# Kernel optimization log

Hardware: AMD Instinct MI355X
Metric: run time of the kernel (lower is better)

Reference implementation:

```python
import jax, jax.numpy as jnp
import numpy as np

BATCH, NUM_BSS, NUM_USERS, M, N = 32, 8, 32, 128, 4
LAGR_ITERS = 8
PSEUDOINV_SVAL_THRESH = 1e-12


def herm(a):
    return 0.5 * (a + jnp.swapaxes(a, -1, -2).conj())


def setup_inputs() -> dict:
    key = jax.random.key(0)
    ks = jax.random.split(key, 7)
    v_re = jax.random.normal(ks[0], (BATCH, NUM_USERS, M, N), jnp.float32)
    v_im = jax.random.normal(ks[1], (BATCH, NUM_USERS, M, N), jnp.float32)
    H_re = jax.random.normal(ks[2], (NUM_BSS, NUM_USERS, N, M), jnp.float32)
    H_im = jax.random.normal(ks[3], (NUM_BSS, NUM_USERS, N, M), jnp.float32)
    noise_pow = jax.random.uniform(ks[4], (BATCH, NUM_USERS), jnp.float32, 0.05, 1.0)
    rweights = jax.random.uniform(ks[5], (BATCH, NUM_USERS), jnp.float32, 0.1, 1.0)
    bss_pow = jnp.ones((BATCH, NUM_BSS), jnp.float32)
    assign = jax.random.randint(ks[6], (NUM_USERS,), 0, NUM_BSS).astype(jnp.int32)
    return {"v_re": v_re, "v_im": v_im, "H_re": H_re, "H_im": H_im,
            "noise_pow": noise_pow, "rweights": rweights, "bss_pow": bss_pow,
            "assign": assign}


def reference(v_re, v_im, H_re, H_im, noise_pow, rweights, bss_pow, assign):
    V = v_re + 1j * v_im          # [B,K,M,N] precoders
    H = H_re + 1j * H_im          # [C,K,N,M] channel BS c -> user k
    K = V.shape[1]
    C = H.shape[0]
    Ndim = V.shape[-1]
    eyeN = jnp.eye(Ndim, dtype=V.dtype)

    # Hg[j, i] = channel from assigned-BS-of-user-j to user i
    Hg = H[assign]                                    # [K,K,N,M]
    # downlink covariance per user i: noise*I + sum_j (H[bs_j,i] V_j)(.)^H
    HV = jnp.einsum('jinm,bjmp->bijnp', Hg, V)        # [B,Ki,Kj,N,N]
    cov = jnp.einsum('bijnp,bijqp->binq', HV, HV.conj())
    cov = herm(cov + noise_pow[..., None, None] * eyeN)
    icov = herm(jnp.linalg.inv(cov))                  # [B,K,N,N]

    idx = jnp.arange(K)
    Hd = Hg[idx, idx]                                 # [K,N,M] direct channels
    HdV = jnp.einsum('knm,bkmp->bknp', Hd, V)         # [B,K,N,N]
    u = jnp.einsum('bknq,bkqp->bknp', icov, HdV)      # receive filters
    w_inv = herm(eyeN - jnp.einsum('bkqn,bkqp->bknp', u.conj(), HdV))
    w = herm(jnp.linalg.inv(w_inv))                   # MSE weights (w_poly=None)
    uwu = herm(jnp.einsum('bknp,bkpq,bkrq->bknr', u, w, u.conj()))
    # v_tilde = H_ii^H u w * rate_weight
    vt = jnp.einsum('knm,bknp,bkpq->bkmq', Hd.conj(), u, w) * rweights[..., None, None]

    # uplink covariance per BS c: sum_k rw_k * H[c,k]^H uwu_k H[c,k]
    ul = herm(jnp.einsum('cknm,bkno,ckop,bk->bcmp', H.conj(), uwu, H, rweights))

    # aux per BS: sum over assigned users of v_tilde v_tilde^H
    Q = jnp.einsum('bkmn,bkpn->bkmp', vt, vt.conj())  # [B,K,M,M]
    aux = jnp.moveaxis(
        jax.ops.segment_sum(jnp.moveaxis(Q, 1, 0), assign, num_segments=C), 0, 1)  # [B,C,M,M]

    lam, E = jnp.linalg.eigh(ul)                      # [B,C,M], [B,C,M,M]
    lam = jnp.maximum(lam, 0.0)
    c = jnp.maximum(jnp.einsum('bcmi,bcmp,bcpi->bci', E.conj(), aux, E).real, 0.0)
    c = c / bss_pow[..., None]

    # solve sum_i c_i/(lam_i+mu)^2 = 1 for mu >= 0 by bisection in [0, sqrt(sum c)]
    hi = jnp.sqrt(jnp.sum(c, -1))
    lo = jnp.zeros_like(hi)
    for _ in range(LAGR_ITERS):
        mid = 0.5 * (lo + hi)
        f = jnp.sum(c / jnp.square(lam + mid[..., None] + 1e-20), -1)
        gt = f > 1.0
        lo = jnp.where(gt, mid, lo)
        hi = jnp.where(gt, hi, mid)
    mu = jnp.maximum(0.5 * (lo + hi), 0.0)            # [B,C]

    # pseudo-inverse of loaded UL covariance via its eigendecomposition
    lam_l = lam + mu[..., None]
    lam_l = jnp.where(lam_l < PSEUDOINV_SVAL_THRESH, 1e12, lam_l)
    inv_aug = herm(jnp.einsum('bcmi,bci,bcni->bcmn', E, 1.0 / lam_l, E.conj()))

    # v update: v_k = inv_aug[assign_k] @ v_tilde_k
    v_out = jnp.einsum('bkmp,bkpn->bkmn', inv_aug[:, assign], vt)  # [B,K,M,N]
    return v_out
```

## Files before the change

kernel.cpp:

```cpp
#include <hip/hip_runtime.h>

#define B_ 32
#define C_ 8
#define K_ 32
#define NCMAX 96
#define BSTR 129

__device__ __forceinline__ float2 cmul(float2 a, float2 b) {
  return make_float2(a.x*b.x - a.y*b.y, a.x*b.y + a.y*b.x);
}
__device__ __forceinline__ float2 cmulc(float2 a, float2 b) {
  return make_float2(a.x*b.x + a.y*b.y, a.y*b.x - a.x*b.y);
}
__device__ __forceinline__ float2 cadd(float2 a, float2 b){ return make_float2(a.x+b.x, a.y+b.y); }
__device__ __forceinline__ float2 csub(float2 a, float2 b){ return make_float2(a.x-b.x, a.y-b.y); }
__device__ __forceinline__ int SK(int r){ return r + ((r >> 3) << 1); }

template<int C>
__device__ __forceinline__ float dppadd(float x) {
  return x + __int_as_float(__builtin_amdgcn_update_dpp(
      0, __float_as_int(x), C, 0xF, 0xF, true));
}
__device__ __forceinline__ float bcast63(float x) {
  return __int_as_float(__builtin_amdgcn_readlane(__float_as_int(x), 63));
}
__device__ __forceinline__ float red4f(float x) {
  x = dppadd<0xB1>(x); return dppadd<0x4E>(x);
}
__device__ __forceinline__ float red16f(float x) {
  x = dppadd<0xB1>(x); x = dppadd<0x4E>(x);
  x = dppadd<0x141>(x); x = dppadd<0x140>(x);
  return x;
}
__device__ __forceinline__ float red64u(float x) {
  x = red16f(x);
  x = dppadd<0x142>(x);
  x = dppadd<0x143>(x);
  return bcast63(x);
}
__device__ __forceinline__ float2 red16c(float2 a){ a.x = red16f(a.x); a.y = red16f(a.y); return a; }
__device__ __forceinline__ float2 red64cu(float2 a){ a.x = red64u(a.x); a.y = red64u(a.y); return a; }

__device__ void herm4_inv(float2 a[4][4], float2 out[4][4]) {
  float idg[4];
  for (int j = 0; j < 4; ++j) {
    float d = sqrtf(fmaxf(a[j][j].x, 1e-30f));
    float id = 1.f / d;
    idg[j] = id;
    a[j][j] = make_float2(d, 0.f);
    for (int r = j+1; r < 4; ++r) { a[r][j].x *= id; a[r][j].y *= id; }
    for (int c = j+1; c < 4; ++c)
      for (int r = c; r < 4; ++r)
        a[r][c] = csub(a[r][c], cmulc(a[r][j], a[c][j]));
  }
  float2 li[4][4];
  for (int j = 0; j < 4; ++j) {
    li[j][j] = make_float2(idg[j], 0.f);
    for (int r = j+1; r < 4; ++r) {
      float2 s = make_float2(0.f, 0.f);
      for (int d = j; d < r; ++d) s = cadd(s, cmul(a[r][d], li[d][j]));
      li[r][j] = make_float2(-s.x*idg[r], -s.y*idg[r]);
    }
  }
  for (int p = 0; p < 4; ++p)
    for (int q = 0; q < 4; ++q) {
      float2 s = make_float2(0.f, 0.f);
      for (int d = (p > q ? p : q); d < 4; ++d)
        s = cadd(s, cmulc(li[d][q], li[d][p]));
      out[p][q] = s;
    }
}

__global__ __launch_bounds__(512, 1) void k_fused(
    const float* __restrict__ v_re, const float* __restrict__ v_im,
    const float* __restrict__ H_re, const float* __restrict__ H_im,
    const float* __restrict__ noise_pow, const float* __restrict__ rweights,
    const float* __restrict__ bss_pow, const int* __restrict__ assign_g,
    void* __restrict__ outp, int omode)
{
  const int t = threadIdx.x;
  const int lane = t & 63, wid = t >> 6;
  const int blk = blockIdx.x;
  const int b = blk >> 3, c = blk & 7;
  const int tm = t >> 4, tp = t & 15;
  const int rbase = tm * 4, cbase = tp * 8;

  __shared__ __align__(16) float2 BsL[NCMAX * BSTR];
  __shared__ __align__(16) float2 Arena[4224];
  __shared__ __align__(16) float2 pS[1024];
  __shared__ __align__(16) float2 dBS2[256];
  __shared__ __align__(16) float2 wS[160];
  __shared__ __align__(16) float2 colS[160];
  __shared__ __align__(16) float2 pvS[128];
  __shared__ __align__(16) float2 tauS[128];
  __shared__ float dS[128], eS[128], cpS[128];
  __shared__ float red[8];
  __shared__ int asg[K_], ulist[K_], nc_s;

  float2* Wall = pS;
  float2* uwS  = pS + 512;
  float2* covS = Arena + 2576;
  float2* HdVS = Arena + 3088;
  float2* Pd   = Arena;
  float2* Tsc  = Arena;
  float2* Vp   = Arena;

  if (t < K_) asg[t] = assign_g[t];
  if (t == 0) {
    int n2 = 0;
    for (int k = 0; k < K_; ++k) if (assign_g[k] == c) ulist[n2++] = k;
    nc_s = n2;
  }
  {
    const int k = t >> 4, n = (t >> 2) & 3, q = t & 3;
    covS[t] = make_float2((n == q) ? noise_pow[b*K_ + k] : 0.f, 0.f);
  }
  __syncthreads();
  const int nc = nc_s;
  if (nc == 0) return;
  const int cols = 4 * nc;
  const int qmax = (cols + 15) >> 4;
  const int passes = (cols + 31) >> 5;

  {
    const int pn = t >> 2, qt = t & 3;
    const int kk = pn >> 2, nn = pn & 3;
    float2* Tb0 = Arena + 1552;
    float2* Tb1 = Arena + 2064;
    for (int j = 0; j < K_; j += 2) {
      #pragma unroll
      for (int bf = 0; bf < 2; ++bf) {
        const int vb = (b*K_ + j + bf) * 512;
        Arena[bf*776 + (t >> 2)*6 + (t & 3) + (t >> 7)*2] =
            make_float2(v_re[vb + t], v_im[vb + t]);
      }
      __syncthreads();
      float2 rr[2][4];
      #pragma unroll
      for (int bf = 0; bf < 2; ++bf) {
        const float2* Vq = Arena + bf*776 + qt*2;
        const int hb = ((asg[j + bf]*K_ + kk)*4 + nn) * 128;
        float2 a0 = {0,0}, a1 = {0,0}, a2 = {0,0}, a3 = {0,0};
        for (int m4 = qt*32; m4 < qt*32 + 32; m4 += 4) {
          const float4 hre = *(const float4*)&H_re[hb + m4];
          const float4 him = *(const float4*)&H_im[hb + m4];
          const float hx[4] = {hre.x, hre.y, hre.z, hre.w};
          const float hy[4] = {him.x, him.y, him.z, him.w};
          #pragma unroll
          for (int i2 = 0; i2 < 4; ++i2) {
            const float4 v01 = *(const float4*)&Vq[(m4 + i2)*6];
            const float4 v23 = *(const float4*)&Vq[(m4 + i2)*6 + 2];
            a0.x += hx[i2]*v01.x - hy[i2]*v01.y; a0.y += hx[i2]*v01.y + hy[i2]*v01.x;
            a1.x += hx[i2]*v01.z - hy[i2]*v01.w; a1.y += hx[i2]*v01.w + hy[i2]*v01.z;
            a2.x += hx[i2]*v23.x - hy[i2]*v23.y; a2.y += hx[i2]*v23.y + hy[i2]*v23.x;
            a3.x += hx[i2]*v23.z - hy[i2]*v23.w; a3.y += hx[i2]*v23.w + hy[i2]*v23.z;
          }
        }
        rr[bf][0] = a0; rr[bf][1] = a1; rr[bf][2] = a2; rr[bf][3] = a3;
      }
      #pragma unroll
      for (int bf = 0; bf < 2; ++bf)
        #pragma unroll
        for (int p = 0; p < 4; ++p) {
          rr[bf][p].x = red4f(rr[bf][p].x);
          rr[bf][p].y = red4f(rr[bf][p].y);
        }
      if (qt == 0) {
        #pragma unroll
        for (int p = 0; p < 4; ++p) {
          Tb0[pn*4 + p] = rr[0][p];
          Tb1[pn*4 + p] = rr[1][p];
        }
      }
      __syncthreads();
      {
        const int k2 = t >> 4, n2 = (t >> 2) & 3, q2 = t & 3;
        float2 acc = covS[t];
        #pragma unroll
        for (int p = 0; p < 4; ++p)
          acc = cadd(acc, cmulc(Tb0[(k2*4 + n2)*4 + p], Tb0[(k2*4 + q2)*4 + p]));
        #pragma unroll
        for (int p = 0; p < 4; ++p)
          acc = cadd(acc, cmulc(Tb1[(k2*4 + n2)*4 + p], Tb1[(k2*4 + q2)*4 + p]));
        covS[t] = acc;
        if (k2 == j)     HdVS[k2*16 + n2*4 + q2] = Tb0[(k2*4 + n2)*4 + q2];
        if (k2 == j + 1) HdVS[k2*16 + n2*4 + q2] = Tb1[(k2*4 + n2)*4 + q2];
      }
      __syncthreads();
    }
  }

  if (t < K_) {
    const int k = t;
    float2 a[4][4], ic[4][4], hv[4][4], u[4][4], wi[4][4], w[4][4], uw[4][4], W[4][4];
    const float rwk = rweights[b*K_ + k];
    for (int r = 0; r < 4; ++r)
      for (int c2 = 0; c2 < 4; ++c2) a[r][c2] = covS[k*16 + r*4 + c2];
    herm4_inv(a, ic);
    for (int r = 0; r < 4; ++r)
      for (int c2 = 0; c2 < 4; ++c2) hv[r][c2] = HdVS[k*16 + r*4 + c2];
    for (int n = 0; n < 4; ++n)
      for (int p = 0; p < 4; ++p) {
        float2 s = {0,0};
        for (int q = 0; q < 4; ++q) s = cadd(s, cmul(ic[n][q], hv[q][p]));
        u[n][p] = s;
      }
    for (int n = 0; n < 4; ++n)
      for (int p = 0; p < 4; ++p) {
        float2 s = make_float2((n == p) ? 1.f : 0.f, 0.f);
        for (int q = 0; q < 4; ++q) s = csub(s, cmulc(hv[q][p], u[q][n]));
        wi[n][p] = s;
      }
    herm4_inv(wi, w);
    for (int n = 0; n < 4; ++n)
      for (int q = 0; q < 4; ++q) {
        float2 s = {0,0};
        for (int p = 0; p < 4; ++p) s = cadd(s, cmul(u[n][p], w[p][q]));
        uw[n][q] = s;
      }
    for (int n = 0; n < 4; ++n)
      for (int r = 0; r < 4; ++r) {
        float2 s = {0,0};
        for (int q = 0; q < 4; ++q) s = cadd(s, cmulc(uw[n][q], u[r][q]));
        W[n][r] = make_float2(s.x * rwk, s.y * rwk);
      }
    for (int n = 0; n < 4; ++n)
      for (int r = n; r < 4; ++r) {
        float2 x1 = W[n][r], x2 = W[r][n];
        float2 hm = make_float2(0.5f*(x1.x + x2.x), 0.5f*(x1.y - x2.y));
        W[n][r] = hm; W[r][n] = make_float2(hm.x, -hm.y);
      }
    for (int idx = 0; idx < 16; ++idx) {
      uwS[k*16 + idx]  = uw[idx >> 2][idx & 3];
      Wall[k*16 + idx] = W[idx >> 2][idx & 3];
    }
  }
  __syncthreads();

  float2 Areg[4][8];
  #pragma unroll
  for (int j = 0; j < 4; ++j)
    #pragma unroll
    for (int cc = 0; cc < 8; ++cc) Areg[j][cc] = make_float2(0.f, 0.f);
  for (int k = 0; k < K_; k += 2) {
    #pragma unroll
    for (int bf = 0; bf < 2; ++bf) {
      const int hb = (c*K_ + k + bf) * 512;
      Arena[bf*520 + (t >> 7)*130 + (t & 127)] = make_float2(H_re[hb + t], H_im[hb + t]);
    }
    __syncthreads();
    #pragma unroll
    for (int bf = 0; bf < 2; ++bf) {
      const int n = t >> 7, p = t & 127;
      const float2* HsB = Arena + bf*520;
      const int kb = (k + bf)*16 + n*4;
      float2 y = {0,0};
      #pragma unroll
      for (int o = 0; o < 4; ++o) y = cadd(y, cmul(Wall[kb + o], HsB[o*130 + p]));
      Arena[1040 + bf*640 + n*160 + p + ((p >> 3) << 1)] = y;
    }
    __syncthreads();
    #pragma unroll
    for (int bf = 0; bf < 2; ++bf) {
      const float2* HsB = Arena + bf*520;
      const float2* YsB = Arena + 1040 + bf*640;
      #pragma unroll
      for (int n = 0; n < 4; ++n) {
        const float4 ha = *(const float4*)&HsB[n*130 + rbase];
        const float4 hc = *(const float4*)&HsB[n*130 + rbase + 2];
        const float2 h0 = make_float2(ha.x, ha.y), h1 = make_float2(ha.z, ha.w);
        const float2 h2 = make_float2(hc.x, hc.y), h3 = make_float2(hc.z, hc.w);
        const float2* yb = &YsB[n*160 + tp*10];
        #pragma unroll
        for (int hq = 0; hq < 2; ++hq) {
          float2 y[4];
          #pragma unroll
          for (int a2 = 0; a2 < 4; a2 += 2) {
            const float4 y4 = *(const float4*)&yb[hq*4 + a2];
            y[a2] = make_float2(y4.x, y4.y); y[a2+1] = make_float2(y4.z, y4.w);
          }
          #pragma unroll
          for (int c4 = 0; c4 < 4; ++c4) {
            const int cc = hq*4 + c4;
            Areg[0][cc].x += h0.x*y[c4].x + h0.y*y[c4].y;
            Areg[0][cc].y += h0.x*y[c4].y - h0.y*y[c4].x;
            Areg[1][cc].x += h1.x*y[c4].x + h1.y*y[c4].y;
            Areg[1][cc].y += h1.x*y[c4].y - h1.y*y[c4].x;
            Areg[2][cc].x += h2.x*y[c4].x + h2.y*y[c4].y;
            Areg[2][cc].y += h2.x*y[c4].y - h2.y*y[c4].x;
            Areg[3][cc].x += h3.x*y[c4].x + h3.y*y[c4].y;
            Areg[3][cc].y += h3.x*y[c4].y - h3.y*y[c4].x;
          }
        }
      }
    }
    __syncthreads();
  }

  float2 Bv[4][8];
  #pragma unroll
  for (int j = 0; j < 4; ++j)
    #pragma unroll
    for (int q = 0; q < 8; ++q) Bv[j][q] = make_float2(0.f, 0.f);
  float trp = 0.f;
  #pragma unroll
  for (int q = 0; q < 8; ++q) {
    const int col = tp + 16*q;
    const int slot = col >> 2, qn = col & 3;
    if (slot < nc) {
      const int k = ulist[slot];
      const float rwk = rweights[b*K_ + k];
      const int hb = (c*K_ + k) * 512;
      float2 acc0 = {0,0}, acc1 = {0,0}, acc2 = {0,0}, acc3 = {0,0};
      #pragma unroll
      for (int n = 0; n < 4; ++n) {
        const float2 uwv = uwS[k*16 + n*4 + qn];
        const float4 hre = *(const float4*)&H_re[hb + n*128 + rbase];
        const float4 him = *(const float4*)&H_im[hb + n*128 + rbase];
        acc0 = cadd(acc0, cmulc(uwv, make_float2(hre.x, him.x)));
        acc1 = cadd(acc1, cmulc(uwv, make_float2(hre.y, him.y)));
        acc2 = cadd(acc2, cmulc(uwv, make_float2(hre.z, him.z)));
        acc3 = cadd(acc3, cmulc(uwv, make_float2(hre.w, him.w)));
      }
      acc0.x *= rwk; acc0.y *= rwk; acc1.x *= rwk; acc1.y *= rwk;
      acc2.x *= rwk; acc2.y *= rwk; acc3.x *= rwk; acc3.y *= rwk;
      Bv[0][q] = acc0; Bv[1][q] = acc1; Bv[2][q] = acc2; Bv[3][q] = acc3;
      trp += acc0.x*acc0.x + acc0.y*acc0.y + acc1.x*acc1.x + acc1.y*acc1.y
           + acc2.x*acc2.x + acc2.y*acc2.y + acc3.x*acc3.x + acc3.y*acc3.y;
    }
  }
  trp = red64u(trp);
  if (lane == 0) red[wid] = trp;
  __syncthreads();
  const float inv_bss = 1.f / bss_pow[b*C_ + c];
  float hi = sqrtf((red[0] + red[1] + red[2] + red[3] +
                    red[4] + red[5] + red[6] + red[7]) * inv_bss);
  float lo = 0.f;

  if (tp == 0) {
    #pragma unroll
    for (int j = 0; j < 4; ++j) colS[SK(rbase + j)] = Areg[j][0];
  }
  __syncthreads();

  #pragma unroll 1
  for (int i = 0; i < 127; ++i) {
    float2 vr[4], vc[8], tau, sc;
    {
      const float2 x0 = colS[SK(lane)], x1 = colS[SK(lane + 64)];
      float sig = 0.f;
      if (lane >= i + 2)      sig += x0.x*x0.x + x0.y*x0.y;
      if (lane + 64 >= i + 2) sig += x1.x*x1.x + x1.y*x1.y;
      sig = red64u(sig);
      const float2 al = colS[SK(i + 1)];
      float beta;
      if (sig <= 1e-30f && fabsf(al.y) <= 1e-30f) {
        beta = al.x; tau = make_float2(0.f, 0.f); sc = make_float2(0.f, 0.f);
      } else {
        const float mag = sqrtf(al.x*al.x + al.y*al.y + sig);
        beta = (al.x >= 0.f) ? -mag : mag;
        const float ib = 1.f / beta;
        tau = make_float2((beta - al.x) * ib, -al.y * ib);
        const float dx = al.x - beta, dy = al.y;
        const float dn = 1.f / (dx*dx + dy*dy);
        sc = make_float2(dx*dn, -dy*dn);
      }
      if (t == 0) { eS[i] = beta; tauS[i] = tau; }
      #pragma unroll
      for (int j = 0; j < 4; ++j) {
        const int r = rbase + j;
        const float2 x = colS[SK(r)];
        vr[j] = (r <= i) ? make_float2(0.f, 0.f)
              : (r == i + 1 ? make_float2(1.f, 0.f) : cmul(x, sc));
      }
      {
        const int cb = SK(cbase);
        const float4 c01 = *(const float4*)&colS[cb];
        const float4 c23 = *(const float4*)&colS[cb + 2];
        const float4 c45 = *(const float4*)&colS[cb + 4];
        const float4 c67 = *(const float4*)&colS[cb + 6];
        const float2 cx[8] = { make_float2(c01.x,c01.y), make_float2(c01.z,c01.w),
                               make_float2(c23.x,c23.y), make_float2(c23.z,c23.w),
                               make_float2(c45.x,c45.y), make_float2(c45.z,c45.w),
                               make_float2(c67.x,c67.y), make_float2(c67.z,c67.w) };
        #pragma unroll
        for (int cc = 0; cc < 8; ++cc) {
          const int r = cbase + cc;
          vc[cc] = (r <= i) ? make_float2(0.f, 0.f)
                 : (r == i + 1 ? make_float2(1.f, 0.f) : cmul(cx[cc], sc));
        }
      }
    }
    {
      float2 part[4];
      #pragma unroll
      for (int j = 0; j < 4; ++j) {
        float2 s = cmul(Areg[j][0], vc[0]);
        #pragma unroll
        for (int cc = 1; cc < 8; ++cc) s = cadd(s, cmul(Areg[j][cc], vc[cc]));
        part[j] = s;
      }
      #pragma unroll
      for (int j = 0; j < 4; ++j) part[j] = red16c(part[j]);
      #pragma unroll
      for (int j = 0; j < 4; ++j) if (tp == j) pvS[rbase + j] = part[j];
      #pragma unroll
      for (int q = 0; q < 8; ++q) {
        if (q >= qmax) continue;
        float2 s = {0.f, 0.f};
        #pragma unroll
        for (int j = 0; j < 4; ++j) s = cadd(s, cmulc(Bv[j][q], vr[j]));
        Pd[tm*130 + tp + 16*q] = s;
      }
    }
    __syncthreads();

    if (wid == 0) {
      float2 p0 = {0.f,0.f}, p1 = {0.f,0.f};
      if (lane > i)      p0 = cmul(tau, pvS[lane]);
      if (lane + 64 > i) p1 = cmul(tau, pvS[lane + 64]);
      float2 v0, v1;
      v0 = (lane <= i) ? make_float2(0.f,0.f)
         : (lane == i + 1 ? make_float2(1.f,0.f) : cmul(colS[SK(lane)], sc));
      { const int r1 = lane + 64;
        v1 = (r1 <= i) ? make_float2(0.f,0.f)
           : (r1 == i + 1 ? make_float2(1.f,0.f) : cmul(colS[SK(r1)], sc)); }
      float2 d0 = cadd(cmulc(p0, v0), cmulc(p1, v1));
      d0 = red64cu(d0);
      const float alr = -0.5f * (tau.x*d0.x + tau.y*d0.y);
      wS[SK(lane)]      = cadd(p0, make_float2(alr*v0.x, alr*v0.y));
      wS[SK(lane + 64)] = cadd(p1, make_float2(alr*v1.x, alr*v1.y));
    } else if (t < 320) {
      const int col = (t - 64) & 127;
      const int half = (t - 64) >> 7;
      float2 s = {0.f, 0.f};
      #pragma unroll
      for (int g = 0; g < 16; ++g) s = cadd(s, Pd[(half*16 + g)*130 + col]);
      dBS2[half*128 + col] = s;
    }
    __syncthreads();

    {
      float2 wr[4], wc[8];
      #pragma unroll
      for (int j = 0; j < 4; ++j) wr[j] = wS[SK(rbase + j)];
      {
        const int cb = SK(cbase);
        const float4 w01 = *(const float4*)&wS[cb];
        const float4 w23 = *(const float4*)&wS[cb + 2];
        const float4 w45 = *(const float4*)&wS[cb + 4];
        const float4 w67 = *(const float4*)&wS[cb + 6];
        wc[0] = make_float2(w01.x,w01.y); wc[1] = make_float2(w01.z,w01.w);
        wc[2] = make_float2(w23.x,w23.y); wc[3] = make_float2(w23.z,w23.w);
        wc[4] = make_float2(w45.x,w45.y); wc[5] = make_float2(w45.z,w45.w);
        wc[6] = make_float2(w67.x,w67.y); wc[7] = make_float2(w67.z,w67.w);
      }
      #pragma unroll
      for (int j = 0; j < 4; ++j)
        #pragma unroll
        for (int cc = 0; cc < 8; ++cc)
          Areg[j][cc] = csub(Areg[j][cc], cadd(cmulc(vr[j], wc[cc]), cmulc(wr[j], vc[cc])));
      const float2 tauc = make_float2(tau.x, -tau.y);
      #pragma unroll
      for (int q = 0; q < 8; ++q) {
        if (q >= qmax) continue;
        const float2 dBt = cmul(tauc, cadd(dBS2[tp + 16*q], dBS2[128 + tp + 16*q]));
        #pragma unroll
        for (int j = 0; j < 4; ++j) Bv[j][q] = csub(Bv[j][q], cmul(dBt, vr[j]));
      }
      if (tp == (i >> 3)) {
        #pragma unroll
        for (int cc = 0; cc < 8; ++cc) if (cc == (i & 7)) {
          #pragma unroll
          for (int j = 0; j < 4; ++j) if (rbase + j >= i + 1) Areg[j][cc] = vr[j];
        }
      }
      if (tp == ((i + 1) >> 3)) {
        #pragma unroll
        for (int cc = 0; cc < 8; ++cc) if (cc == ((i + 1) & 7)) {
          #pragma unroll
          for (int j = 0; j < 4; ++j) colS[SK(rbase + j)] = Areg[j][cc];
        }
      }
    }
    __syncthreads();
  }

  if (tp == (tm >> 1)) {
    const int co = (tm & 1) * 4;
    #pragma unroll
    for (int j = 0; j < 4; ++j)
      #pragma unroll
      for (int cc = 0; cc < 8; ++cc)
        if (cc == co + j) dS[rbase + j] = Areg[j][cc].x;
  }
  #pragma unroll
  for (int q = 0; q < 8; ++q) {
    const int col = tp + 16*q;
    if ((col >> 2) < nc) {
      #pragma unroll
      for (int j = 0; j < 4; ++j) BsL[col*BSTR + rbase + j] = Bv[j][q];
    }
  }
  __syncthreads();

  if (wid == 0) {
    for (int it = 0; it <= 8; ++it) {
      const float mu = 0.5f * (lo + hi);
      float fsum = 0.f;
      for (int p = 0; p < passes; ++p) {
        const int colg = 32*p + (lane & 31);
        const bool act = (lane < 32) && (colg < cols);
        float2* Bcol = BsL + colg*BSTR;
        float m = dS[0] + mu;
        float im = 1.f / m;
        float2 g = act ? Bcol[0] : make_float2(0.f, 0.f);
        g.x *= im; g.y *= im;
        if (act) Tsc[lane] = g;
        float cp = eS[0] * im;
        if (lane == 0) cpS[0] = cp;
        #pragma unroll 4
        for (int r = 1; r < 128; ++r) {
          const float e0 = eS[r-1];
          m = dS[r] + mu - e0 * cp;
          im = 1.f / m;
          float2 gr = act ? Bcol[r] : make_float2(0.f, 0.f);
          gr.x = (gr.x - e0 * g.x) * im;
          gr.y = (gr.y - e0 * g.y) * im;
          g = gr;
          if (act) Tsc[r*33 + lane] = gr;
          if (r < 127) { cp = eS[r] * im; if (lane == 0) cpS[r] = cp; }
        }
        float2 z = g;
        float acc = z.x*z.x + z.y*z.y;
        if (it == 8 && act) Bcol[127] = z;
        #pragma unroll 4
        for (int r = 126; r >= 0; --r) {
          const float cpr = cpS[r];
          const float2 gp = act ? Tsc[r*33 + lane] : make_float2(0.f, 0.f);
          z.x = gp.x - cpr * z.x;
          z.y = gp.y - cpr * z.y;
          acc += z.x*z.x + z.y*z.y;
          if (it == 8 && act) Bcol[r] = z;
        }
        if (act) fsum += acc;
      }
      if (it < 8) {
        fsum = red64u(fsum);
        const float f = fsum * inv_bss;
        if (f > 1.0f) lo = mu; else hi = mu;
      }
    }
  }
  __syncthreads();

  for (int base = 0; base < cols; base += 32) {
    float2 z0[4], z1[4];
    bool act[4];
    #pragma unroll
    for (int qq = 0; qq < 4; ++qq) {
      const int col = base + wid + 8*qq;
      act[qq] = (col < cols);
      const int cc2 = act[qq] ? col : 0;
      z0[qq] = BsL[cc2*BSTR + lane];
      z1[qq] = BsL[cc2*BSTR + lane + 64];
    }
    for (int P = 7; P >= 0; --P) {
      const int p0i = P * 16;
      const int smax = (P == 7) ? 14 : 15;
      __syncthreads();
      if (tp == 2*P) {
        #pragma unroll
        for (int s = 0; s < 8; ++s) {
          const int ii = p0i + s;
          #pragma unroll
          for (int j = 0; j < 4; ++j) {
            const int r = rbase + j;
            Vp[(s << 7) + r] = (r >= ii + 1) ? Areg[j][s] : make_float2(0.f, 0.f);
          }
        }
      }
      if (tp == 2*P + 1) {
        #pragma unroll
        for (int s = 8; s < 16; ++s) {
          if (s > smax) continue;
          const int ii = p0i + s;
          #pragma unroll
          for (int j = 0; j < 4; ++j) {
            const int r = rbase + j;
            Vp[(s << 7) + r] = (r >= ii + 1) ? Areg[j][s - 8] : make_float2(0.f, 0.f);
          }
        }
      }
      __syncthreads();
      for (int s = smax; s >= 0; --s) {
        const float2 tv = tauS[p0i + s];
        const float2 v0 = Vp[(s << 7) + lane];
        const float2 v1 = Vp[(s << 7) + lane + 64];
        float2 d[4];
        #pragma unroll
        for (int qq = 0; qq < 4; ++qq) {
          d[qq] = cadd(cmulc(z0[qq], v0), cmulc(z1[qq], v1));
          d[qq] = red64cu(d[qq]);
        }
        #pragma unroll
        for (int qq = 0; qq < 4; ++qq) {
          const float2 td = cmul(tv, d[qq]);
          z0[qq] = csub(z0[qq], cmul(td, v0));
          z1[qq] = csub(z1[qq], cmul(td, v1));
        }
      }
    }
    #pragma unroll
    for (int qq = 0; qq < 4; ++qq) if (act[qq]) {
      const int col = base + wid + 8*qq;
      const int slotc = col >> 2, qn = col & 3;
      const int k = ulist[slotc];
      const size_t obase = (size_t)(b*K_ + k) * 512;
      const size_t oe0 = obase + (size_t)lane*4 + qn;
      const size_t oe1 = obase + (size_t)(lane + 64)*4 + qn;
      if (omode == 0) {
        ((float2*)outp)[oe0] = z0[qq];
        ((float2*)outp)[oe1] = z1[qq];
      } else {
        ((float*)outp)[oe0] = z0[qq].x;
        ((float*)outp)[oe1] = z1[qq].x;
      }
    }
  }
}

extern "C" void kernel_launch(void* const* d_in, const int* in_sizes, int n_in,
                              void* d_out, int out_size, void* d_ws, size_t ws_size,
                              hipStream_t stream)
{
  (void)in_sizes; (void)n_in; (void)d_ws; (void)ws_size;
  const float* v_re   = (const float*)d_in[0];
  const float* v_im   = (const float*)d_in[1];
  const float* H_re   = (const float*)d_in[2];
  const float* H_im   = (const float*)d_in[3];
  const float* noise  = (const float*)d_in[4];
  const float* rw     = (const float*)d_in[5];
  const float* bss    = (const float*)d_in[6];
  const int*   assign = (const int*)d_in[7];

  const int omode = (out_size == B_*K_*128*4) ? 1 : 0;

  hipLaunchKernelGGL(k_fused, dim3(B_*C_), dim3(512), 0, stream,
                     v_re, v_im, H_re, H_im, noise, rw, bss, assign, d_out, omode);
}
```

Before: 1.216 ms.

## Redistribute B columns per wavefront to apply Householder updates with wave reductions

Moves the RHS matrix B (applied alongside the Householder tridiagonalization) from a 4-row by 8-column per-thread tile to a layout where each wavefront holds whole columns, two rows per lane. Each reflector update then becomes a 64-lane reduction plus an in-register rank-1 update. This removes the partial-sum scratch array, the cross-thread summation pass in threads 64-319 and its shared-memory round trips. The cost is up to 8 serial wave reductions per wavefront in every one of the 127 iterations.

```diff
diff --git a/kernel.cpp b/kernel.cpp
--- a/kernel.cpp
+++ b/kernel.cpp
@@ -88,7 +88,6 @@
   __shared__ __align__(16) float2 BsL[NCMAX * BSTR];
   __shared__ __align__(16) float2 Arena[4224];
   __shared__ __align__(16) float2 pS[1024];
-  __shared__ __align__(16) float2 dBS2[256];
   __shared__ __align__(16) float2 wS[160];
   __shared__ __align__(16) float2 colS[160];
   __shared__ __align__(16) float2 pvS[128];
@@ -101,7 +100,6 @@
   float2* uwS  = pS + 512;
   float2* covS = Arena + 2576;
   float2* HdVS = Arena + 3088;
-  float2* Pd   = Arena;
   float2* Tsc  = Arena;
   float2* Vp   = Arena;
 
@@ -119,7 +117,6 @@
   const int nc = nc_s;
   if (nc == 0) return;
   const int cols = 4 * nc;
-  const int qmax = (cols + 15) >> 4;
   const int passes = (cols + 31) >> 5;
 
   {
@@ -297,36 +294,30 @@
     __syncthreads();
   }
 
-  float2 Bv[4][8];
+  float2 Bw0[8], Bw1[8];
   #pragma unroll
-  for (int j = 0; j < 4; ++j)
-    #pragma unroll
-    for (int q = 0; q < 8; ++q) Bv[j][q] = make_float2(0.f, 0.f);
+  for (int qq = 0; qq < 8; ++qq) { Bw0[qq] = make_float2(0.f,0.f); Bw1[qq] = make_float2(0.f,0.f); }
   float trp = 0.f;
   #pragma unroll
-  for (int q = 0; q < 8; ++q) {
-    const int col = tp + 16*q;
-    const int slot = col >> 2, qn = col & 3;
-    if (slot < nc) {
+  for (int qq = 0; qq < 8; ++qq) {
+    const int col = wid + 8*qq;
+    if (col < cols) {
+      const int slot = col >> 2, qn = col & 3;
       const int k = ulist[slot];
       const float rwk = rweights[b*K_ + k];
       const int hb = (c*K_ + k) * 512;
-      float2 acc0 = {0,0}, acc1 = {0,0}, acc2 = {0,0}, acc3 = {0,0};
+      float2 a0 = {0,0}, a1 = {0,0};
       #pragma unroll
       for (int n = 0; n < 4; ++n) {
         const float2 uwv = uwS[k*16 + n*4 + qn];
-        const float4 hre = *(const float4*)&H_re[hb + n*128 + rbase];
-        const float4 him = *(const float4*)&H_im[hb + n*128 + rbase];
-        acc0 = cadd(acc0, cmulc(uwv, make_float2(hre.x, him.x)));
-        acc1 = cadd(acc1, cmulc(uwv, make_float2(hre.y, him.y)));
-        acc2 = cadd(acc2, cmulc(uwv, make_float2(hre.z, him.z)));
-        acc3 = cadd(acc3, cmulc(uwv, make_float2(hre.w, him.w)));
-      }
-      acc0.x *= rwk; acc0.y *= rwk; acc1.x *= rwk; acc1.y *= rwk;
-      acc2.x *= rwk; acc2.y *= rwk; acc3.x *= rwk; acc3.y *= rwk;
-      Bv[0][q] = acc0; Bv[1][q] = acc1; Bv[2][q] = acc2; Bv[3][q] = acc3;
-      trp += acc0.x*acc0.x + acc0.y*acc0.y + acc1.x*acc1.x + acc1.y*acc1.y
-           + acc2.x*acc2.x + acc2.y*acc2.y + acc3.x*acc3.x + acc3.y*acc3.y;
+        a0 = cadd(a0, cmulc(uwv, make_float2(H_re[hb + n*128 + lane],
+                                             H_im[hb + n*128 + lane])));
+        a1 = cadd(a1, cmulc(uwv, make_float2(H_re[hb + n*128 + lane + 64],
+                                             H_im[hb + n*128 + lane + 64])));
+      }
+      a0.x *= rwk; a0.y *= rwk; a1.x *= rwk; a1.y *= rwk;
+      Bw0[qq] = a0; Bw1[qq] = a1;
+      trp += a0.x*a0.x + a0.y*a0.y + a1.x*a1.x + a1.y*a1.y;
     }
   }
   trp = red64u(trp);
@@ -345,7 +336,7 @@
 
   #pragma unroll 1
   for (int i = 0; i < 127; ++i) {
-    float2 vr[4], vc[8], tau, sc;
+    float2 vr[4], vc[8], v0, v1, tau, sc;
     {
       const float2 x0 = colS[SK(lane)], x1 = colS[SK(lane + 64)];
       float sig = 0.f;
@@ -366,6 +357,11 @@
         sc = make_float2(dx*dn, -dy*dn);
       }
       if (t == 0) { eS[i] = beta; tauS[i] = tau; }
+      v0 = (lane <= i) ? make_float2(0.f,0.f)
+         : (lane == i + 1 ? make_float2(1.f,0.f) : cmul(x0, sc));
+      { const int r1 = lane + 64;
+        v1 = (r1 <= i) ? make_float2(0.f,0.f)
+           : (r1 == i + 1 ? make_float2(1.f,0.f) : cmul(x1, sc)); }
       #pragma unroll
       for (int j = 0; j < 4; ++j) {
         const int r = rbase + j;
@@ -404,13 +400,16 @@
       for (int j = 0; j < 4; ++j) part[j] = red16c(part[j]);
       #pragma unroll
       for (int j = 0; j < 4; ++j) if (tp == j) pvS[rbase + j] = part[j];
-      #pragma unroll
-      for (int q = 0; q < 8; ++q) {
-        if (q >= qmax) continue;
-        float2 s = {0.f, 0.f};
-        #pragma unroll
-        for (int j = 0; j < 4; ++j) s = cadd(s, cmulc(Bv[j][q], vr[j]));
-        Pd[tm*130 + tp + 16*q] = s;
+      const float2 tauc = make_float2(tau.x, -tau.y);
+      #pragma unroll
+      for (int qq = 0; qq < 8; ++qq) {
+        const int col = wid + 8*qq;
+        if (col >= cols) continue;
+        float2 d = cadd(cmulc(Bw0[qq], v0), cmulc(Bw1[qq], v1));
+        d = red64cu(d);
+        const float2 dBt = cmul(tauc, d);
+        Bw0[qq] = csub(Bw0[qq], cmul(dBt, v0));
+        Bw1[qq] = csub(Bw1[qq], cmul(dBt, v1));
       }
     }
     __syncthreads();
@@ -419,24 +418,11 @@
       float2 p0 = {0.f,0.f}, p1 = {0.f,0.f};
       if (lane > i)      p0 = cmul(tau, pvS[lane]);
       if (lane + 64 > i) p1 = cmul(tau, pvS[lane + 64]);
-      float2 v0, v1;
-      v0 = (lane <= i) ? make_float2(0.f,0.f)
-         : (lane == i + 1 ? make_float2(1.f,0.f) : cmul(colS[SK(lane)], sc));
-      { const int r1 = lane + 64;
-        v1 = (r1 <= i) ? make_float2(0.f,0.f)
-           : (r1 == i + 1 ? make_float2(1.f,0.f) : cmul(colS[SK(r1)], sc)); }
       float2 d0 = cadd(cmulc(p0, v0), cmulc(p1, v1));
       d0 = red64cu(d0);
       const float alr = -0.5f * (tau.x*d0.x + tau.y*d0.y);
       wS[SK(lane)]      = cadd(p0, make_float2(alr*v0.x, alr*v0.y));
       wS[SK(lane + 64)] = cadd(p1, make_float2(alr*v1.x, alr*v1.y));
-    } else if (t < 320) {
-      const int col = (t - 64) & 127;
-      const int half = (t - 64) >> 7;
-      float2 s = {0.f, 0.f};
-      #pragma unroll
-      for (int g = 0; g < 16; ++g) s = cadd(s, Pd[(half*16 + g)*130 + col]);
-      dBS2[half*128 + col] = s;
     }
     __syncthreads();
 
@@ -460,14 +446,6 @@
         #pragma unroll
         for (int cc = 0; cc < 8; ++cc)
           Areg[j][cc] = csub(Areg[j][cc], cadd(cmulc(vr[j], wc[cc]), cmulc(wr[j], vc[cc])));
-      const float2 tauc = make_float2(tau.x, -tau.y);
-      #pragma unroll
-      for (int q = 0; q < 8; ++q) {
-        if (q >= qmax) continue;
-        const float2 dBt = cmul(tauc, cadd(dBS2[tp + 16*q], dBS2[128 + tp + 16*q]));
-        #pragma unroll
-        for (int j = 0; j < 4; ++j) Bv[j][q] = csub(Bv[j][q], cmul(dBt, vr[j]));
-      }
       if (tp == (i >> 3)) {
         #pragma unroll
         for (int cc = 0; cc < 8; ++cc) if (cc == (i & 7)) {
@@ -495,11 +473,11 @@
         if (cc == co + j) dS[rbase + j] = Areg[j][cc].x;
   }
   #pragma unroll
-  for (int q = 0; q < 8; ++q) {
-    const int col = tp + 16*q;
-    if ((col >> 2) < nc) {
-      #pragma unroll
-      for (int j = 0; j < 4; ++j) BsL[col*BSTR + rbase + j] = Bv[j][q];
+  for (int qq = 0; qq < 8; ++qq) {
+    const int col = wid + 8*qq;
+    if (col < cols) {
+      BsL[col*BSTR + lane]      = Bw0[qq];
+      BsL[col*BSTR + lane + 64] = Bw1[qq];
     }
   }
   __syncthreads();
@@ -595,19 +573,19 @@
       __syncthreads();
       for (int s = smax; s >= 0; --s) {
         const float2 tv = tauS[p0i + s];
-        const float2 v0 = Vp[(s << 7) + lane];
-        const float2 v1 = Vp[(s << 7) + lane + 64];
+        const float2 v0b = Vp[(s << 7) + lane];
+        const float2 v1b = Vp[(s << 7) + lane + 64];
         float2 d[4];
         #pragma unroll
         for (int qq = 0; qq < 4; ++qq) {
-          d[qq] = cadd(cmulc(z0[qq], v0), cmulc(z1[qq], v1));
+          d[qq] = cadd(cmulc(z0[qq], v0b), cmulc(z1[qq], v1b));
           d[qq] = red64cu(d[qq]);
         }
         #pragma unroll
         for (int qq = 0; qq < 4; ++qq) {
           const float2 td = cmul(tv, d[qq]);
-          z0[qq] = csub(z0[qq], cmul(td, v0));
-          z1[qq] = csub(z1[qq], cmul(td, v1));
+          z0[qq] = csub(z0[qq], cmul(td, v0b));
+          z1[qq] = csub(z1[qq], cmul(td, v1b));
         }
       }
     }
```

After: 1.181 ms (median of 2 runs). 1.03x faster.
